# Kernel tuning notes

Hardware: AMD Instinct MI355X
Metric: run time of the kernel (lower is better)

Reference implementation:

```python
import jax, jax.numpy as jnp
import numpy as np
from jax.scipy.special import erf

# ---- static config (mirrors module __init__) ----
G = 64          # graphs per batch
N = 64          # atoms per graph (equal-size graphs)
T = G * N       # total atoms
NUM_TYPES = 4
DEG = 32        # avg neighbors per atom
E = T * DEG
F = 128         # node feature dim
R_MAX = 6.0
R_IN = 1.0
EPS = 0.5       # fill value for distance matrix / cross-graph gamma
Q_TOT = 0.0


def setup_inputs() -> dict:
    key = jax.random.key(0)
    ks = jax.random.split(key, 12)
    batch = jnp.repeat(jnp.arange(G, dtype=jnp.int64), N)
    types = jax.random.randint(ks[0], (T,), 0, NUM_TYPES)
    node_attrs = jax.nn.one_hot(types, NUM_TYPES, dtype=jnp.float32)
    # within-graph random edges, symmetrized
    src = jax.random.randint(ks[1], (E // 2,), 0, T)
    dst = (src // N) * N + jax.random.randint(ks[2], (E // 2,), 0, N)
    edge_index = jnp.stack([jnp.concatenate([src, dst]),
                            jnp.concatenate([dst, src])]).astype(jnp.int64)
    half_len = jax.random.uniform(ks[3], (E // 2,), minval=1.0, maxval=R_MAX, dtype=jnp.float32)
    edge_length = jnp.concatenate([half_len, half_len])[:, None]
    kappa = jax.random.normal(ks[4], (T,), dtype=jnp.float32)
    node_feats = jax.random.normal(ks[5], (T, F), dtype=jnp.float32)
    ref_eta = jax.random.uniform(ks[6], (NUM_TYPES,), minval=0.5, maxval=1.5, dtype=jnp.float32)
    ref_log_sigma = jax.random.normal(ks[7], (NUM_TYPES,), dtype=jnp.float32) * 0.1
    ref_A = jax.random.uniform(ks[8], (NUM_TYPES, NUM_TYPES), minval=10.0, maxval=50.0, dtype=jnp.float32)
    ref_B = jax.random.uniform(ks[9], (NUM_TYPES, NUM_TYPES), minval=2.0, maxval=4.0, dtype=jnp.float32)
    ref_C = jax.random.uniform(ks[10], (NUM_TYPES, NUM_TYPES), minval=100.0, maxval=300.0, dtype=jnp.float32)
    ref_D = jnp.zeros((NUM_TYPES, NUM_TYPES), dtype=jnp.float32)
    ref_mu = jax.random.uniform(ks[11], (NUM_TYPES, NUM_TYPES), minval=0.8, maxval=1.2, dtype=jnp.float32)
    # symmetrize pairwise refs (type-pair parameters)
    sym = lambda m: 0.5 * (m + m.T)
    short_energy = jax.random.normal(jax.random.fold_in(key, 100), (G, 1), dtype=jnp.float32)
    atomic_short_energy = jax.random.normal(jax.random.fold_in(key, 101), (T, 1), dtype=jnp.float32)
    return dict(batch=batch, node_attrs=node_attrs, edge_index=edge_index,
                edge_length=edge_length, kappa=kappa, node_feats=node_feats,
                ref_eta=ref_eta, ref_log_sigma=ref_log_sigma,
                ref_A=sym(ref_A), ref_B=sym(ref_B), ref_C=sym(ref_C),
                ref_D=ref_D, ref_mu=sym(ref_mu),
                short_energy=short_energy, atomic_short_energy=atomic_short_energy)


def _f_cut(R):
    c1 = jnp.tanh(1.0) ** 3
    in1 = (R > 0.0) & (R < R_IN)
    in2 = (R >= R_IN) & (R <= R_MAX)
    smooth = jnp.tanh(1.0 - (R - R_IN) / (R_MAX - R_IN)) ** 3
    return jnp.where(in1, c1, jnp.where(in2, smooth, 0.0))


def reference(batch, node_attrs, edge_index, edge_length, kappa, node_feats,
              ref_eta, ref_log_sigma, ref_A, ref_B, ref_C, ref_D, ref_mu,
              short_energy, atomic_short_energy):
    types = jnp.argmax(node_attrs, axis=1)              # [T]
    ref_sigma = jnp.exp(ref_log_sigma)
    sigma = ref_sigma[types]                            # [T]
    eta = ref_eta[types]                                # [T]
    ref_gamma = jnp.sqrt(ref_sigma[:, None] ** 2 + ref_sigma[None, :] ** 2)
    same = batch[:, None] == batch[None, :]             # [T,T] block mask
    tij = (types[:, None], types[None, :])
    gamma = jnp.where(same, ref_gamma[tij], EPS)

    # dense distance matrix: eps fill, edge distances scattered in
    R = jnp.full((T, T), EPS, dtype=jnp.float32)
    R = R.at[edge_index[0], edge_index[1]].set(edge_length[:, 0])
    Fc = _f_cut(R)

    factor = erf(R / (jnp.sqrt(2.0) * gamma)) / R       # [T,T]
    sqrt_pi = jnp.sqrt(jnp.pi).astype(jnp.float32)
    A_ij = jnp.diag(eta + 1.0 / (sigma * sqrt_pi)) + factor
    A_tril = jnp.tril(A_ij)

    # per-graph diagonal blocks -> extended (N+1) charge-equilibration solve
    A4 = A_tril.reshape(G, N, G, N)
    g = jnp.arange(G)
    A_blocks = A4[g, :, g, :]                           # [G,N,N]
    A_ext = jnp.zeros((G, N + 1, N + 1), dtype=jnp.float32)
    A_ext = A_ext.at[:, :N, :N].set(A_blocks)
    A_ext = A_ext.at[:, N, :N].set(1.0).at[:, :N, N].set(1.0)
    kappa_ext = jnp.concatenate([kappa.reshape(G, N),
                                 jnp.full((G, 1), Q_TOT, dtype=jnp.float32)], axis=1)
    sol = jnp.linalg.solve(A_ext, -kappa_ext[..., None])[..., 0]  # [G,N+1]
    charges = sol[:, :N].reshape(T)                     # drop Lagrange multiplier

    atomic_potentials = (factor * Fc) @ charges         # [T]
    E_factor = jnp.diag(0.5 / (sigma * sqrt_pi)) + factor
    V = E_factor @ charges
    atomic_E_el = charges * V                           # [T]
    E_el = jax.ops.segment_sum(atomic_E_el, batch, num_segments=G)[:, None]

    # two-body short-range repulsion/dispersion
    pair = lambda ref: jnp.where(same, ref[tij], 0.0)
    Am, Bm, Cm, Dm, mum = pair(ref_A), pair(ref_B), pair(ref_C), pair(ref_D), pair(ref_mu)
    E2b_ij = (Am * jnp.exp(Bm * (mum - R)) - Cm / R ** 6 - Dm / R ** 8) * Fc
    E2b_ij = E2b_ij * (1.0 - jnp.eye(T, dtype=jnp.float32))
    atomic_E2b = (E2b_ij.sum(axis=-1) * 0.5)[:, None]   # [T,1]
    E_2b = jax.ops.segment_sum(atomic_E2b, batch, num_segments=G)  # [G,1]

    E_tot = E_el + E_2b + short_energy                  # [G,1]
    node_energy = atomic_E_el[:, None] + atomic_E2b + atomic_short_energy
    node_feats_out = jnp.concatenate([node_feats, charges[:, None],
                                      atomic_potentials[:, None]], axis=1)
    return E_tot, node_energy, charges, node_feats_out
```

## Files before the change

kernel.cpp:

```cpp
#include <hip/hip_runtime.h>

#define G 64
#define TT 4096
#define EDGES 131072
#define HALF 65536

#define OUT_ETOT 0
#define OUT_NODEE 64
#define OUT_Q (64 + 4096)
#define OUT_NF (64 + 4096 + 4096)

typedef unsigned long long ull;

__device__ __forceinline__ float wave_sum_f(float v) {
#pragma unroll
    for (int m = 1; m < 64; m <<= 1) v += __shfl_xor(v, m);
    return v;
}
__device__ __forceinline__ double wave_sum_d(double v) {
#pragma unroll
    for (int m = 1; m < 64; m <<= 1) v += __shfl_xor(v, m);
    return v;
}
__device__ __forceinline__ double bcast_d(double v, int j) {
    union { double d; int i[2]; } u;
    u.d = v;
    union { int i[2]; double d; } r;
    r.i[0] = __builtin_amdgcn_readlane(u.i[0], j);
    r.i[1] = __builtin_amdgcn_readlane(u.i[1], j);
    return r.d;
}
__device__ __forceinline__ int type_of(float4 na) {
    int t = 0;
    float best = na.x;
    if (na.y > best) { best = na.y; t = 1; }
    if (na.z > best) { best = na.z; t = 2; }
    if (na.w > best) { best = na.w; t = 3; }
    return t;
}
__device__ __forceinline__ float fcut(float R, float c1) {
    if (R < 1.0f) return c1;
    if (R > 6.0f) return 0.0f;
    float x = 1.0f - (R - 1.0f) * 0.2f;
    float ex = __expf(2.0f * x);
    float t = (ex - 1.0f) / (ex + 1.0f);
    return t * t * t;
}

__global__ __launch_bounds__(1024, 1) void k_main(
    const int* __restrict__ ei, const float* __restrict__ elen,
    const float* __restrict__ node_attrs, const float* __restrict__ kappa,
    const float* __restrict__ ref_eta, const float* __restrict__ ref_log_sigma,
    const float* __restrict__ ref_A, const float* __restrict__ ref_B,
    const float* __restrict__ ref_C, const float* __restrict__ ref_D,
    const float* __restrict__ ref_mu, const float* __restrict__ short_e,
    const float* __restrict__ atomic_short, const float* __restrict__ nf_in,
    float* __restrict__ out) {
    __shared__ ull s_pack[4096];
    __shared__ float sL[64][65];
    __shared__ float sF[64][65];
    __shared__ float s_diag[64];
    __shared__ float s_q[64];
    __shared__ float s_ash[64];
    __shared__ float s_red[16];

    const int g = blockIdx.x;
    const int tid = threadIdx.x;
    const int lane = tid & 63;
    const int wv = tid >> 6;
    const float SQRT_PI = 1.7724538509055159f;
    const float th1 = tanhf(1.0f);
    const float c1 = th1 * th1 * th1;

#pragma unroll
    for (int k = 0; k < 4; ++k) s_pack[tid + k * 1024] = 0ull;
    const float4 na = *(const float4*)(node_attrs + ((size_t)((g << 6) + lane) << 2));
    const int tj = type_of(na);
    const float sgj = __expf(ref_log_sigma[tj]);
    if (tid < 64) {
        s_diag[tid] = ref_eta[tj] + 1.0f / (sgj * SQRT_PI);
        s_ash[tid] = atomic_short[(g << 6) + tid];
    }
    __syncthreads();

    {
        const int4* src4 = (const int4*)ei;
        const int4* dst4 = (const int4*)(ei + EDGES);
        const float4* len4 = (const float4*)elen;
#pragma unroll 2
        for (int b = tid; b < HALF / 4; b += 1024) {
            const int4 si = src4[b];
            const int4 dj = dst4[b];
            const float4 rr = len4[b];
            const int e0 = b << 2;
            int iv[4] = { si.x, si.y, si.z, si.w };
            int jv[4] = { dj.x, dj.y, dj.z, dj.w };
            float Rv[4] = { rr.x, rr.y, rr.z, rr.w };
#pragma unroll
            for (int k = 0; k < 4; ++k) {
                if ((iv[k] >> 6) == g) {
                    const ull rb = (ull)__float_as_uint(Rv[k]);
                    const int e = e0 + k;
                    atomicMax(&s_pack[((iv[k] & 63) << 6) + (jv[k] & 63)],
                              ((ull)(unsigned)e << 32) | rb);
                    atomicMax(&s_pack[((jv[k] & 63) << 6) + (iv[k] & 63)],
                              ((ull)(unsigned)(e + HALF) << 32) | rb);
                }
            }
        }
    }
    __syncthreads();

    float e2b[4];
#pragma unroll
    for (int r = 0; r < 4; ++r) {
        const int row = (wv << 2) + r;
        const ull pk = s_pack[(row << 6) + lane];
        const int ti = __shfl(tj, row);
        const float sgi = __shfl(sgj, row);
        const float gam = sqrtf(sgi * sgi + sgj * sgj);
        const float R = (pk > 0ull) ? __uint_as_float((unsigned)pk) : 0.5f;
        const float rinv = __frcp_rn(R);
        const float factor = erff(R * (0.70710678118654752f / gam)) * rinv;
        const float fc = fcut(R, c1);
        sL[row][lane] = factor;
        sF[row][lane] = factor * fc;
        float e = 0.0f;
        if (row != lane) {
            int t4 = ti * 4 + tj;
            float r2 = rinv * rinv;
            float r6 = r2 * r2 * r2;
            e = (ref_A[t4] * __expf(ref_B[t4] * (ref_mu[t4] - R)) -
                 ref_C[t4] * r6 - ref_D[t4] * (r6 * r2)) * fc;
        }
        e2b[r] = e;
    }
#pragma unroll
    for (int m = 1; m < 64; m <<= 1) {
#pragma unroll
        for (int r = 0; r < 4; ++r) e2b[r] += __shfl_xor(e2b[r], m);
    }
    __syncthreads();

    if (wv == 0) {
        const int i = tid;
        double Ld = (double)(s_diag[i] + sL[i][i]);
        double inv = 1.0 / Ld;
        double au = 1.0;
        double av = (double)kappa[(g << 6) + i];
        double my_u = 0.0, my_v = 0.0;
        for (int j = 0; j < 64; ++j) {
            double ij = bcast_d(inv, j);
            double uj = bcast_d(au, j) * ij;
            double vj = bcast_d(av, j) * ij;
            if (i == j) { my_u = uj; my_v = vj; }
            if (i > j) {
                double Lij = (double)sL[i][j];
                au -= Lij * uj;
                av -= Lij * vj;
            }
        }
        double Su = wave_sum_d(my_u);
        double Sv = wave_sum_d(my_v);
        double lam = Sv / Su;
        s_q[i] = (float)(-my_v + lam * my_u);
    } else {
        for (int t2 = tid - 64; t2 < 4096; t2 += 960) {
            int row = t2 >> 6, c = t2 & 63;
            float2 v = ((const float2*)nf_in)[(((g << 6) + row) << 6) + c];
            *(float2*)(out + OUT_NF + (size_t)((g << 6) + row) * 130 + c * 2) = v;
        }
    }
    __syncthreads();

    const float qj = s_q[lane];
    float pr[4], wr[4];
#pragma unroll
    for (int r = 0; r < 4; ++r) {
        const int row = (wv << 2) + r;
        pr[r] = sF[row][lane] * qj;
        wr[r] = sL[row][lane] * qj;
    }
#pragma unroll
    for (int m = 1; m < 64; m <<= 1) {
#pragma unroll
        for (int r = 0; r < 4; ++r) {
            pr[r] += __shfl_xor(pr[r], m);
            wr[r] += __shfl_xor(wr[r], m);
        }
    }
    float acc = 0.0f;
#pragma unroll
    for (int r = 0; r < 4; ++r) {
        const int row = (wv << 2) + r;
        const float q = s_q[row];
        const float sgi = __shfl(sgj, row);
        if (lane == 0) {
            float coef = 0.5f / (sgi * SQRT_PI);
            float aEel = q * (wr[r] + coef * q);
            float e2 = 0.5f * e2b[r];
            out[OUT_NODEE + (g << 6) + row] = aEel + e2 + s_ash[row];
            out[OUT_Q + (g << 6) + row] = q;
            size_t nfb = OUT_NF + (size_t)((g << 6) + row) * 130;
            out[nfb + 128] = q;
            out[nfb + 129] = pr[r];
            acc += aEel + e2;
        }
    }
    if (lane == 0) s_red[wv] = acc;
    __syncthreads();
    if (tid == 0) {
        float s = 0.0f;
#pragma unroll
        for (int k = 0; k < 16; ++k) s += s_red[k];
        out[OUT_ETOT + g] = s + short_e[g];
    }
}

extern "C" void kernel_launch(void* const* d_in, const int* in_sizes, int n_in,
                              void* d_out, int out_size, void* d_ws, size_t ws_size,
                              hipStream_t stream) {
    const float* node_attrs = (const float*)d_in[1];
    const int* edge_index = (const int*)d_in[2];
    const float* edge_length = (const float*)d_in[3];
    const float* kappa = (const float*)d_in[4];
    const float* node_feats = (const float*)d_in[5];
    const float* ref_eta = (const float*)d_in[6];
    const float* ref_log_sigma = (const float*)d_in[7];
    const float* ref_A = (const float*)d_in[8];
    const float* ref_B = (const float*)d_in[9];
    const float* ref_C = (const float*)d_in[10];
    const float* ref_D = (const float*)d_in[11];
    const float* ref_mu = (const float*)d_in[12];
    const float* short_energy = (const float*)d_in[13];
    const float* atomic_short = (const float*)d_in[14];

    k_main<<<G, 1024, 0, stream>>>(edge_index, edge_length, node_attrs, kappa,
                                   ref_eta, ref_log_sigma, ref_A, ref_B, ref_C,
                                   ref_D, ref_mu, short_energy, atomic_short,
                                   node_feats, (float*)d_out);
}
```

Baseline: 28.70 us.

## Split kernel into solve stage and wide per-atom energy/potential stage

The single 64-block kernel becomes two launches. The first block per graph scatters edges, builds the Coulomb matrix, runs the serial Cholesky-like solve for charges, and writes the packed distance matrix and charges to workspace. A second kernel with 1024 blocks then computes the two-body energies, potentials and outputs per atom, and accumulates graph energies with atomicAdd. This moves the epilogue work off the critical path of the occupancy-limited first kernel, at the cost of an extra launch, a global round-trip of 2 MB of packed data, and float atomics that make the summation order nondeterministic. It also raises the unroll factor on the edge scan.

```diff
diff --git a/kernel.cpp b/kernel.cpp
--- a/kernel.cpp
+++ b/kernel.cpp
@@ -47,30 +47,22 @@
     return t * t * t;
 }
 
-__global__ __launch_bounds__(1024, 1) void k_main(
+__global__ __launch_bounds__(1024, 1) void k_part1(
     const int* __restrict__ ei, const float* __restrict__ elen,
     const float* __restrict__ node_attrs, const float* __restrict__ kappa,
     const float* __restrict__ ref_eta, const float* __restrict__ ref_log_sigma,
-    const float* __restrict__ ref_A, const float* __restrict__ ref_B,
-    const float* __restrict__ ref_C, const float* __restrict__ ref_D,
-    const float* __restrict__ ref_mu, const float* __restrict__ short_e,
-    const float* __restrict__ atomic_short, const float* __restrict__ nf_in,
+    const float* __restrict__ short_e, const float* __restrict__ nf_in,
+    ull* __restrict__ packed_g, float* __restrict__ qc,
     float* __restrict__ out) {
     __shared__ ull s_pack[4096];
     __shared__ float sL[64][65];
-    __shared__ float sF[64][65];
     __shared__ float s_diag[64];
-    __shared__ float s_q[64];
-    __shared__ float s_ash[64];
-    __shared__ float s_red[16];
 
     const int g = blockIdx.x;
     const int tid = threadIdx.x;
     const int lane = tid & 63;
     const int wv = tid >> 6;
     const float SQRT_PI = 1.7724538509055159f;
-    const float th1 = tanhf(1.0f);
-    const float c1 = th1 * th1 * th1;
 
 #pragma unroll
     for (int k = 0; k < 4; ++k) s_pack[tid + k * 1024] = 0ull;
@@ -79,15 +71,15 @@
     const float sgj = __expf(ref_log_sigma[tj]);
     if (tid < 64) {
         s_diag[tid] = ref_eta[tj] + 1.0f / (sgj * SQRT_PI);
-        s_ash[tid] = atomic_short[(g << 6) + tid];
-    }
+    }
+    if (tid == 64) out[OUT_ETOT + g] = short_e[g];
     __syncthreads();
 
     {
         const int4* src4 = (const int4*)ei;
         const int4* dst4 = (const int4*)(ei + EDGES);
         const float4* len4 = (const float4*)elen;
-#pragma unroll 2
+#pragma unroll 4
         for (int b = tid; b < HALF / 4; b += 1024) {
             const int4 si = src4[b];
             const int4 dj = dst4[b];
@@ -111,34 +103,14 @@
     }
     __syncthreads();
 
-    float e2b[4];
 #pragma unroll
     for (int r = 0; r < 4; ++r) {
         const int row = (wv << 2) + r;
         const ull pk = s_pack[(row << 6) + lane];
-        const int ti = __shfl(tj, row);
         const float sgi = __shfl(sgj, row);
         const float gam = sqrtf(sgi * sgi + sgj * sgj);
         const float R = (pk > 0ull) ? __uint_as_float((unsigned)pk) : 0.5f;
-        const float rinv = __frcp_rn(R);
-        const float factor = erff(R * (0.70710678118654752f / gam)) * rinv;
-        const float fc = fcut(R, c1);
-        sL[row][lane] = factor;
-        sF[row][lane] = factor * fc;
-        float e = 0.0f;
-        if (row != lane) {
-            int t4 = ti * 4 + tj;
-            float r2 = rinv * rinv;
-            float r6 = r2 * r2 * r2;
-            e = (ref_A[t4] * __expf(ref_B[t4] * (ref_mu[t4] - R)) -
-                 ref_C[t4] * r6 - ref_D[t4] * (r6 * r2)) * fc;
-        }
-        e2b[r] = e;
-    }
-#pragma unroll
-    for (int m = 1; m < 64; m <<= 1) {
-#pragma unroll
-        for (int r = 0; r < 4; ++r) e2b[r] += __shfl_xor(e2b[r], m);
+        sL[row][lane] = erff(R * (0.70710678118654752f / gam)) * __frcp_rn(R);
     }
     __syncthreads();
 
@@ -163,57 +135,84 @@
         double Su = wave_sum_d(my_u);
         double Sv = wave_sum_d(my_v);
         double lam = Sv / Su;
-        s_q[i] = (float)(-my_v + lam * my_u);
+        qc[(g << 6) + i] = (float)(-my_v + lam * my_u);
     } else {
+        for (int t = tid - 64; t < 4096; t += 960)
+            packed_g[((size_t)g << 12) + t] = s_pack[t];
         for (int t2 = tid - 64; t2 < 4096; t2 += 960) {
             int row = t2 >> 6, c = t2 & 63;
             float2 v = ((const float2*)nf_in)[(((g << 6) + row) << 6) + c];
             *(float2*)(out + OUT_NF + (size_t)((g << 6) + row) * 130 + c * 2) = v;
         }
     }
-    __syncthreads();
-
-    const float qj = s_q[lane];
-    float pr[4], wr[4];
-#pragma unroll
-    for (int r = 0; r < 4; ++r) {
-        const int row = (wv << 2) + r;
-        pr[r] = sF[row][lane] * qj;
-        wr[r] = sL[row][lane] * qj;
-    }
+}
+
+__global__ __launch_bounds__(256) void k_part2(
+    const ull* __restrict__ packed_g, const float* __restrict__ qc,
+    const float* __restrict__ node_attrs,
+    const float* __restrict__ ref_log_sigma, const float* __restrict__ ref_A,
+    const float* __restrict__ ref_B, const float* __restrict__ ref_C,
+    const float* __restrict__ ref_D, const float* __restrict__ ref_mu,
+    const float* __restrict__ atomic_short, float* __restrict__ out) {
+    __shared__ float s_red[4];
+    const int wv = threadIdx.x >> 6;
+    const int i = blockIdx.x * 4 + wv;
+    const int lane = threadIdx.x & 63;
+    const int g = i >> 6;
+    const int ir = i & 63;
+    const float SQRT_PI = 1.7724538509055159f;
+    const float th1 = tanhf(1.0f);
+    const float c1 = th1 * th1 * th1;
+
+    const ull pk = packed_g[((size_t)i << 6) + lane];
+    const float qj = qc[(g << 6) + lane];
+    const float4 na = *(const float4*)(node_attrs + ((size_t)((g << 6) + lane) << 2));
+
+    const int tj = type_of(na);
+    const int ti = __shfl(tj, ir);
+    const float sgj = __expf(ref_log_sigma[tj]);
+    const float sgi = __shfl(sgj, ir);
+    const float gam = sqrtf(sgi * sgi + sgj * sgj);
+
+    const float R = (pk > 0ull) ? __uint_as_float((unsigned)pk) : 0.5f;
+    const float rinv = __frcp_rn(R);
+    const float factor = erff(R * (0.70710678118654752f / gam)) * rinv;
+    const float fc = fcut(R, c1);
+
+    float e = 0.0f;
+    if (ir != lane) {
+        int t4 = ti * 4 + tj;
+        float r2 = rinv * rinv;
+        float r6 = r2 * r2 * r2;
+        e = (ref_A[t4] * __expf(ref_B[t4] * (ref_mu[t4] - R)) -
+             ref_C[t4] * r6 - ref_D[t4] * (r6 * r2)) * fc;
+    }
+    float p = factor * fc * qj;
+    float w = factor * qj;
 #pragma unroll
     for (int m = 1; m < 64; m <<= 1) {
-#pragma unroll
-        for (int r = 0; r < 4; ++r) {
-            pr[r] += __shfl_xor(pr[r], m);
-            wr[r] += __shfl_xor(wr[r], m);
-        }
-    }
-    float acc = 0.0f;
-#pragma unroll
-    for (int r = 0; r < 4; ++r) {
-        const int row = (wv << 2) + r;
-        const float q = s_q[row];
-        const float sgi = __shfl(sgj, row);
-        if (lane == 0) {
-            float coef = 0.5f / (sgi * SQRT_PI);
-            float aEel = q * (wr[r] + coef * q);
-            float e2 = 0.5f * e2b[r];
-            out[OUT_NODEE + (g << 6) + row] = aEel + e2 + s_ash[row];
-            out[OUT_Q + (g << 6) + row] = q;
-            size_t nfb = OUT_NF + (size_t)((g << 6) + row) * 130;
-            out[nfb + 128] = q;
-            out[nfb + 129] = pr[r];
-            acc += aEel + e2;
-        }
-    }
-    if (lane == 0) s_red[wv] = acc;
-    __syncthreads();
-    if (tid == 0) {
-        float s = 0.0f;
-#pragma unroll
-        for (int k = 0; k < 16; ++k) s += s_red[k];
-        out[OUT_ETOT + g] = s + short_e[g];
+        p += __shfl_xor(p, m);
+        w += __shfl_xor(w, m);
+        e += __shfl_xor(e, m);
+    }
+    const float q = __shfl(qj, ir);
+
+    if (lane == 0) {
+        float aE2b = 0.5f * e;
+        float coef = 0.5f / (sgi * SQRT_PI);
+        float V = w + coef * q;
+        float aEel = q * V;
+        out[OUT_NODEE + i] = aEel + aE2b + atomic_short[i];
+        out[OUT_Q + i] = q;
+        size_t nfb = OUT_NF + (size_t)i * 130;
+        out[nfb + 128] = q;
+        out[nfb + 129] = p;
+        s_red[wv] = aEel + aE2b;
+    }
+    __syncthreads();
+    if (threadIdx.x == 0) {
+        atomicAdd(&out[OUT_ETOT + g],
+                  s_red[0] + s_red[1] + s_red[2] + s_red[3]);
     }
 }
 
@@ -235,8 +234,14 @@
     const float* short_energy = (const float*)d_in[13];
     const float* atomic_short = (const float*)d_in[14];
 
-    k_main<<<G, 1024, 0, stream>>>(edge_index, edge_length, node_attrs, kappa,
-                                   ref_eta, ref_log_sigma, ref_A, ref_B, ref_C,
-                                   ref_D, ref_mu, short_energy, atomic_short,
-                                   node_feats, (float*)d_out);
-}
+    float* out = (float*)d_out;
+    ull* packed_g = (ull*)d_ws;
+    float* qc = (float*)((char*)d_ws + (2u << 20));
+
+    k_part1<<<G, 1024, 0, stream>>>(edge_index, edge_length, node_attrs, kappa,
+                                    ref_eta, ref_log_sigma, short_energy,
+                                    node_feats, packed_g, qc, out);
+    k_part2<<<TT / 4, 256, 0, stream>>>(packed_g, qc, node_attrs,
+                                        ref_log_sigma, ref_A, ref_B, ref_C,
+                                        ref_D, ref_mu, atomic_short, out);
+}
```

After: 34.05 us. +18.6%, slower.
